# Kernel optimization log

Measured on AMD Instinct MI355X. Metric: run time of the kernel, lower is better.

The kernel has to match this reference:

```python
import math
import jax, jax.numpy as jnp
import numpy as np
from jax import lax

EPS = 1e-6
SAMPLE_RATIO = 0.25
K = 5


def _grid_idx(loc_orig, h, w):
    # loc_orig in [-1,1] -> nearest grid cell flat index (row-major)
    loc = (jnp.clip(loc_orig, -1.0, 1.0) + 1.0) * 0.5
    col = jnp.clip(jnp.round(loc[..., 0] * (w - 1)).astype(jnp.int32), 0, w - 1)
    row = jnp.clip(jnp.round(loc[..., 1] * (h - 1)).astype(jnp.int32), 0, h - 1)
    return row * w + col


def token2map(x, loc_orig, idx_agg, H, W):
    # scatter tokens (via their original points) into an HxW grid, averaging per cell
    B, N, C = x.shape
    N0 = idx_agg.shape[1]
    idx_hw = _grid_idx(loc_orig, H, W)                      # (B, N0)
    tok = jax.vmap(lambda xb, ib: xb[ib])(x, idx_agg)       # (B, N0, C)

    def per_b(ihw, t):
        cnt = jax.ops.segment_sum(jnp.ones((N0,), x.dtype), ihw, num_segments=H * W)
        s = jax.ops.segment_sum(t, ihw, num_segments=H * W)
        return s / (cnt + EPS)[:, None]

    grid = jax.vmap(per_b)(idx_hw, tok)                     # (B, H*W, C)
    return grid.reshape(B, H, W, C).transpose(0, 3, 1, 2)   # (B, C, H, W)


def map2token(x_map, N, loc_orig, idx_agg, agg_weight):
    # gather map values at original points, weighted scatter-reduce back to N tokens
    B, C, h, w = x_map.shape
    idx_hw = _grid_idx(loc_orig, h, w)
    flat = x_map.reshape(B, C, h * w).transpose(0, 2, 1)    # (B, hw, C)
    feat = jax.vmap(lambda fb, ib: fb[ib])(flat, idx_hw)    # (B, N0, C)
    aw = agg_weight[..., 0]                                 # (B, N0)

    def per_b(ia, a, f):
        tot = jax.ops.segment_sum(a, ia, num_segments=N) + EPS
        return jax.ops.segment_sum(f * (a / tot[ia])[:, None], ia, num_segments=N)

    return jax.vmap(per_b)(idx_agg, aw, feat)               # (B, N, C)


def cluster_dpc_knn(x, cluster_num, k):
    # DPC-KNN: density from k-NN distances, parent distance, score = dist*density
    B, N, C = x.shape
    sq = jnp.sum(x * x, -1)
    dist = jnp.sqrt(jnp.maximum(sq[:, :, None] + sq[:, None, :]
                                - 2.0 * jnp.einsum('bnc,bmc->bnm', x, x), 0.0)) / math.sqrt(C)
    neg_near, _ = lax.top_k(-dist, k)                       # k nearest (incl. self, dist 0)
    density = jnp.exp(-jnp.mean(jnp.square(neg_near), -1))  # (B, N)
    mask = density[:, None, :] > density[:, :, None]
    dist_max = jnp.max(dist.reshape(B, -1), -1)[:, None, None]
    d_parent = jnp.min(jnp.where(mask, dist, dist_max), -1)
    score = d_parent * density
    _, index_down = lax.top_k(score, cluster_num)           # (B, M) cluster centers
    dist_down = jax.vmap(lambda db, ib: db[ib])(dist, index_down)  # (B, M, N)
    idx_cluster = jnp.argmin(dist_down, axis=1)             # (B, N)
    b = jnp.arange(B)[:, None]
    idx_cluster = idx_cluster.at[b, index_down].set(jnp.arange(cluster_num)[None, :])
    return idx_cluster


def layer_norm(x, g, b):
    mu = jnp.mean(x, -1, keepdims=True)
    xc = x - mu
    return xc * lax.rsqrt(jnp.mean(xc * xc, -1, keepdims=True) + 1e-5) * g + b


def setup_inputs() -> dict:
    key = jax.random.key(0)
    ks = jax.random.split(key, 8)
    B, N, C, DOUT, H, W = 4, 4096, 128, 256, 64, 64
    return {
        "x": jax.random.normal(ks[0], (B, N, C), jnp.float32),
        "loc_orig": jax.random.uniform(ks[1], (B, N, 2), jnp.float32, minval=-1.0, maxval=1.0),
        "idx_agg": jax.random.randint(ks[2], (B, N), 0, N),
        "agg_weight": jax.random.uniform(ks[3], (B, N, 1), jnp.float32),
        "H": H,
        "W": W,
        "idx_k_loc": jax.random.randint(ks[4], (B, N, K), 0, N),
        "conv_w": jax.random.normal(ks[5], (DOUT, C, 3, 3), jnp.float32) * 0.02,
        "conv_b": jnp.zeros((DOUT,), jnp.float32),
        "skip_w": jax.random.normal(ks[6], (DOUT, C), jnp.float32) * 0.02,
        "ln_g": jnp.ones((DOUT,), jnp.float32),
        "ln_b": jnp.zeros((DOUT,), jnp.float32),
        "conf_w": jax.random.normal(ks[7], (1, DOUT), jnp.float32) * 0.02,
        "conf_b": jnp.zeros((1,), jnp.float32),
    }


def reference(x, loc_orig, idx_agg, agg_weight, H, W, idx_k_loc,
              conv_w, conv_b, skip_w, ln_g, ln_b, conf_w, conf_b):
    B, N, C = x.shape
    x_map = token2map(x, loc_orig, idx_agg, H, W)           # (B, C, H, W)
    x_map = lax.conv_general_dilated(x_map, conv_w, (2, 2), ((1, 1), (1, 1)),
                                     dimension_numbers=('NCHW', 'OIHW', 'NCHW'))
    x_map = x_map + conv_b[None, :, None, None]             # (B, DOUT, H/2, W/2)
    xt = map2token(x_map, N, loc_orig, idx_agg, agg_weight) + x @ skip_w.T
    xt = layer_norm(xt, ln_g, ln_b)
    conf = xt @ conf_w.T + conf_b                           # (B, N, 1)
    weight = jnp.exp(conf)[..., 0]                          # (B, N)
    M = max(int(math.ceil(N * SAMPLE_RATIO)), 1)
    idx_cluster = cluster_dpc_knn(xt, M, K)                 # (B, N)

    def merge_b(ic, wb, xb):
        allw = jax.ops.segment_sum(wb, ic, num_segments=M) + EPS
        nw = wb / allw[ic]
        return jax.ops.segment_sum(xb * nw[:, None], ic, num_segments=M), nw

    x_down, norm_w = jax.vmap(merge_b)(idx_cluster, weight, xt)   # (B, M, DOUT), (B, N)
    idx_agg_down = jax.vmap(lambda ic, ia: ic[ia])(idx_cluster, idx_agg)        # (B, N0)
    weight_t = jax.vmap(lambda nw, ia: nw[ia])(norm_w, idx_agg)[..., None]      # (B, N0, 1)
    agg_weight_down = agg_weight * weight_t
    agg_weight_down = agg_weight_down / jnp.max(agg_weight_down, axis=1, keepdims=True)
    # down_block treated as identity (external module); use_grid=False path -> idx_k_loc_down is None
    return (x_down, idx_agg_down, agg_weight_down)
```

## Files before the change

### kernel.cpp

```cpp
#include <hip/hip_runtime.h>
#include <math.h>

#define NB 4
#define NT 4096
#define CI 128
#define DOUT 256
#define HWI 4096
#define HWO 1024
#define MC 1024
#define EPS_F 1e-6f
#define GSZ 16777216ull
#define GSZB 67108864ull

typedef unsigned short u16;
typedef __attribute__((ext_vector_type(8))) short bf16x8;
typedef __attribute__((ext_vector_type(4))) float f32x4;

static const size_t OFF_XMAP  = 0;
static const size_t OFF_CNT   = OFF_XMAP + 8388608;
static const size_t OFF_TOT   = OFF_CNT  + 65536;
static const size_t OFF_ALLW  = OFF_TOT  + 65536;
static const size_t OFF_VMAX  = OFF_ALLW + 16384;
static const size_t OFF_AWDM  = OFF_VMAX + 256;
static const size_t ZERO_BYTES= OFF_AWDM + 256;
static const size_t OFF_YMAP  = ZERO_BYTES;
static const size_t OFF_XT    = OFF_YMAP + 4194304;
static const size_t OFF_SQ    = OFF_XT + 16777216;
static const size_t OFF_DEN   = OFF_SQ + 65536;
static const size_t OFF_SCORE = OFF_DEN + 65536;
static const size_t OFF_WT    = OFF_SCORE + 65536;
static const size_t OFF_AWD   = OFF_WT + 65536;
static const size_t OFF_IDXD  = OFF_AWD + 65536;
static const size_t OFF_IDXC  = OFF_IDXD + 16384;
static const size_t OFF_INV   = OFF_IDXC + 65536;
static const size_t OFF_WTR   = OFF_INV + 65536;
static const size_t OFF_SWT   = OFF_WTR + 1179648;
static const size_t OFF_P     = OFF_SWT + 131072;
static const size_t OFF_XH    = OFF_P + 18874368;
static const size_t OFF_XM    = OFF_XH + 8388608;
static const size_t OFF_XL    = OFF_XM + 8388608;
static const size_t OFF_G     = OFF_XL + 8388608;
static const size_t DPSTRIDE  = (size_t)NT*32*6;

__device__ __forceinline__ float waveSum(float v){
#pragma unroll
  for (int m = 1; m < 64; m <<= 1) v += __shfl_xor(v, m, 64);
  return v;
}
__device__ __forceinline__ float blockSum256(float v, float* red){
  v = waveSum(v);
  int lane = threadIdx.x & 63, wid = threadIdx.x >> 6;
  __syncthreads();
  if (lane == 0) red[wid] = v;
  __syncthreads();
  return red[0] + red[1] + red[2] + red[3];
}
__device__ __forceinline__ void merge5(float& a0, float& a1, float& a2, float& a3, float& a4,
                                       float b0, float b1, float b2, float b3, float b4){
  float l0=a0,l1=a1,l2=a2,l3=fminf(a3,b4),l4=fminf(a4,b3),l5=b2,l6=b1,l7=b0;
  float t0=fminf(l0,l4), t4=fmaxf(l0,l4);
  float t1=fminf(l1,l5), t5=fmaxf(l1,l5);
  float t2=fminf(l2,l6), t6=fmaxf(l2,l6);
  float t3=fminf(l3,l7), t7=fmaxf(l3,l7);
  float u0=fminf(t0,t2), u2=fmaxf(t0,t2);
  float u1=fminf(t1,t3), u3=fmaxf(t1,t3);
  float u4=fminf(t4,t6);
  float u5=fminf(t5,t7);
  a0=fminf(u0,u1); a1=fmaxf(u0,u1);
  a2=fminf(u2,u3); a3=fmaxf(u2,u3);
  a4=fminf(u4,u5);
}
__device__ __forceinline__ void ins5(float v, float& t0, float& t1, float& t2, float& t3, float& t4){
  t4 = fminf(t4, v);
  float a;
  a = fminf(t3,t4); t4 = fmaxf(t3,t4); t3 = a;
  a = fminf(t2,t3); t3 = fmaxf(t2,t3); t2 = a;
  a = fminf(t1,t2); t2 = fmaxf(t1,t2); t1 = a;
  a = fminf(t0,t1); t1 = fmaxf(t0,t1); t0 = a;
}
__device__ __forceinline__ int grid_cell(float lx, float ly, int dim){
  lx = (fminf(fmaxf(lx, -1.f), 1.f) + 1.f) * 0.5f;
  ly = (fminf(fmaxf(ly, -1.f), 1.f) + 1.f) * 0.5f;
  float s = (float)(dim - 1);
  int col = (int)rintf(lx * s); col = min(max(col, 0), dim - 1);
  int row = (int)rintf(ly * s); row = min(max(row, 0), dim - 1);
  return row * dim + col;
}

__global__ __launch_bounds__(256) void t2m_scatter(const float* __restrict__ x,
                                                   const float* __restrict__ loc,
                                                   const int* __restrict__ idx_agg,
                                                   const float* __restrict__ aggw,
                                                   float* __restrict__ xmap, float* __restrict__ cnt,
                                                   float* __restrict__ tot){
  int lin = blockIdx.x * 256 + threadIdx.x;
  int c  = lin & 127;
  int bn = lin >> 7;
  int b  = bn >> 12;
  float lx = loc[(size_t)bn*2 + 0];
  float ly = loc[(size_t)bn*2 + 1];
  int cell = grid_cell(lx, ly, 64);
  int ia = idx_agg[bn];
  float val = x[((size_t)(b*NT + ia))*CI + c];
  atomicAdd(&xmap[((size_t)(b*HWI + cell))*CI + c], val);
  if (c == 0) atomicAdd(&cnt[b*HWI + cell], 1.0f);
  if (c == 1) atomicAdd(&tot[b*NT + ia], aggw[bn]);
}

__global__ __launch_bounds__(256) void wprep_kernel(const float* __restrict__ cw, const float* __restrict__ sw,
                                                    float* __restrict__ wT, float* __restrict__ swT){
  int lin = blockIdx.x * 256 + threadIdx.x;
  if (lin < 1152*256){
    int k = lin >> 8, d = lin & 255;
    wT[lin] = cw[(size_t)d*1152 + k];
  } else {
    int i = lin - 1152*256;
    int c = i >> 8, d = i & 255;
    swT[i] = sw[d*128 + c];
  }
}

__global__ __launch_bounds__(256) void im2col_kernel(const float* __restrict__ xmap,
                                                     const float* __restrict__ cnt,
                                                     float* __restrict__ P){
  int tid = threadIdx.x;
  int c = tid & 127, n2 = tid >> 7;
  int n = blockIdx.x * 2 + n2;
  int b = n >> 10, rem = n & 1023;
  int oh = rem >> 5, ow = rem & 31;
  const float* xb = xmap + (size_t)b*HWI*CI;
  const float* cb_ = cnt + (size_t)b*HWI;
  float* prow = P + (size_t)n*1152 + c*9;
#pragma unroll
  for (int kh = 0; kh < 3; ++kh){
    int ih = oh*2 - 1 + kh;
#pragma unroll
    for (int kw = 0; kw < 3; ++kw){
      int iw = ow*2 - 1 + kw;
      bool inb = (ih >= 0) && (ih < 64) && (iw >= 0) && (iw < 64);
      float v = 0.f;
      if (inb){
        int cell = ih*64 + iw;
        v = xb[(size_t)cell*CI + c] / (cb_[cell] + EPS_F);
      }
      prow[kh*3 + kw] = v;
    }
  }
}

__global__ __launch_bounds__(256) void conv_gemm(const float* __restrict__ P,
                                                 const float* __restrict__ wT,
                                                 const float* __restrict__ cb,
                                                 float* __restrict__ ymap){
  __shared__ float As[16][64];
  __shared__ float Bs[16][32];
  int n0 = blockIdx.x * 64, d0 = blockIdx.y * 32;
  int tid = threadIdx.x;
  int tx = tid & 15, ty = tid >> 4;
  int ln = tid & 63, kq = tid >> 6;
  int bkr = tid >> 3, bc4 = (tid & 7) * 4;
  float4 pav = *(const float4*)(P + (size_t)(n0+ln)*1152 + kq*4);
  float4 pbv;
  if (tid < 128) pbv = *(const float4*)(wT + (size_t)bkr*256 + d0 + bc4);
  float acc[4][2] = {{0}};
  for (int kt = 0; kt < 72; ++kt){
    __syncthreads();
    As[kq*4+0][ln]=pav.x; As[kq*4+1][ln]=pav.y; As[kq*4+2][ln]=pav.z; As[kq*4+3][ln]=pav.w;
    if (tid < 128) *(float4*)&Bs[bkr][bc4] = pbv;
    __syncthreads();
    if (kt < 71){
      int k2 = (kt + 1) * 16;
      pav = *(const float4*)(P + (size_t)(n0+ln)*1152 + k2 + kq*4);
      if (tid < 128) pbv = *(const float4*)(wT + (size_t)(k2 + bkr)*256 + d0 + bc4);
    }
#pragma unroll
    for (int k = 0; k < 16; ++k){
      float ar[4];
      *(float4*)ar = *(const float4*)&As[k][ty*4];
      float b0 = Bs[k][tx*2], b1 = Bs[k][tx*2+1];
#pragma unroll
      for (int r = 0; r < 4; ++r){ acc[r][0] += ar[r]*b0; acc[r][1] += ar[r]*b1; }
    }
  }
  float c0 = cb[d0 + tx*2], c1 = cb[d0 + tx*2 + 1];
#pragma unroll
  for (int r = 0; r < 4; ++r){
    float2 o; o.x = acc[r][0] + c0; o.y = acc[r][1] + c1;
    *(float2*)(ymap + (size_t)(n0 + ty*4 + r)*DOUT + d0 + tx*2) = o;
  }
}

__global__ __launch_bounds__(256) void skip_kernel(const float* __restrict__ x,
                                                   const float* __restrict__ swT,
                                                   float* __restrict__ xt){
  int rowbase = blockIdx.x * 8;
  int d = threadIdx.x;
  __shared__ float xr[8*128];
  ((float4*)xr)[d] = ((const float4*)(x + (size_t)rowbase*CI))[d];
  __syncthreads();
  float acc[8] = {0,0,0,0,0,0,0,0};
  for (int c = 0; c < 128; ++c){
    float w = swT[c*256 + d];
#pragma unroll
    for (int r = 0; r < 8; ++r) acc[r] += w * xr[r*128 + c];
  }
  for (int r = 0; r < 8; ++r) xt[(size_t)(rowbase + r)*DOUT + d] = acc[r];
}

__global__ __launch_bounds__(256) void m2t_scatter(const float* __restrict__ ymap,
                                                   const float* __restrict__ loc,
                                                   const int* __restrict__ idx_agg,
                                                   const float* __restrict__ aggw,
                                                   const float* __restrict__ tot,
                                                   float* __restrict__ xt){
  int bn = blockIdx.x;
  int d = threadIdx.x;
  int b = bn >> 12;
  float lx = loc[(size_t)bn*2 + 0];
  float ly = loc[(size_t)bn*2 + 1];
  int cell = grid_cell(lx, ly, 32);
  int ia = idx_agg[bn];
  float w = aggw[bn] / (tot[b*NT + ia] + EPS_F);
  float val = ymap[((size_t)(b*HWO + cell))*DOUT + d] * w;
  atomicAdd(&xt[((size_t)(b*NT + ia))*DOUT + d], val);
}

__global__ __launch_bounds__(256) void ln_kernel(float* __restrict__ xt,
                                                 const float* __restrict__ g,
                                                 const float* __restrict__ bta,
                                                 const float* __restrict__ cw,
                                                 const float* __restrict__ cb,
                                                 float* __restrict__ sq, float* __restrict__ wt){
  __shared__ float red[4];
  int row = blockIdx.x;
  int d = threadIdx.x;
  float v = xt[(size_t)row*DOUT + d];
  float mu = blockSum256(v, red) * (1.0f/256.0f);
  float xc = v - mu;
  float var = blockSum256(xc*xc, red) * (1.0f/256.0f);
  float rn = 1.0f / sqrtf(var + 1e-5f);
  float y = xc * rn * g[d] + bta[d];
  xt[(size_t)row*DOUT + d] = y;
  float s2 = blockSum256(y*y, red);
  float cf = blockSum256(y*cw[d], red);
  if (d == 0){ sq[row] = s2; wt[row] = expf(cf + cb[0]); }
}

__global__ __launch_bounds__(256) void xsplit_kernel(const float* __restrict__ xt,
                                                     u16* __restrict__ xh,
                                                     u16* __restrict__ xm,
                                                     u16* __restrict__ xl){
  int idx = blockIdx.x*256 + threadIdx.x;
  float2 v = *(const float2*)(xt + (size_t)idx*2);
  unsigned ph, pm, pl;
  {
    unsigned u = __float_as_uint(v.x);
    unsigned h0 = u >> 16;
    float r1 = v.x - __uint_as_float(u & 0xFFFF0000u);
    unsigned u1 = __float_as_uint(r1);
    unsigned m0 = u1 >> 16;
    float r2 = r1 - __uint_as_float(u1 & 0xFFFF0000u);
    unsigned l0 = __float_as_uint(r2) >> 16;
    unsigned u2 = __float_as_uint(v.y);
    unsigned h1 = u2 >> 16;
    float s1 = v.y - __uint_as_float(u2 & 0xFFFF0000u);
    unsigned u3 = __float_as_uint(s1);
    unsigned m1 = u3 >> 16;
    float s2 = s1 - __uint_as_float(u3 & 0xFFFF0000u);
    unsigned l1 = __float_as_uint(s2) >> 16;
    ph = h0 | (h1 << 16); pm = m0 | (m1 << 16); pl = l0 | (l1 << 16);
  }
  *(unsigned*)(xh + (size_t)idx*2) = ph;
  *(unsigned*)(xm + (size_t)idx*2) = pm;
  *(unsigned*)(xl + (size_t)idx*2) = pl;
}

__global__ __launch_bounds__(256) void gram_mfma(const u16* __restrict__ xh,
                                                 const u16* __restrict__ xm,
                                                 const u16* __restrict__ xl,
                                                 const float* __restrict__ sq,
                                                 float* __restrict__ G,
                                                 float* __restrict__ Dpart,
                                                 int b_base, size_t gstride){
  __shared__ u16 usmem[24576];
  u16* Au = usmem;
  u16* Bu = usmem + 12288;
  int b = b_base + blockIdx.y;
  float* Gb = G + (size_t)blockIdx.y*gstride;
  float* Dp = Dpart + (size_t)blockIdx.y*DPSTRIDE;
  int t = blockIdx.x;
  int ti = 0, accu = 0;
  while (accu + ti + 1 <= t){ accu += ti + 1; ++ti; }
  int tj = t - accu;
  int i0 = ti*128, j0 = tj*128;
  int tid = threadIdx.x;
  int w = tid >> 6, l = tid & 63;
  int lrow = l & 15, lg = l >> 4;
  const size_t base = (size_t)b*NT*256;
  const u16* csrc[3] = {xh, xm, xl};
  const u16* gptr[12];
  u16* lptr[12];
  {
    int ci = 0;
#pragma unroll
    for (int side = 0; side < 2; ++side)
#pragma unroll
      for (int c = 0; c < 3; ++c)
#pragma unroll
        for (int wv = 0; wv < 2; ++wv){
          int win = w + wv*4;
          int s = win*64 + l;
          int r = (s >> 3) * 2;
          int g = s ^ (r & 7);
          if ((g >> 2) != r){ r += 1; g = s ^ (r & 7); }
          int q = g & 3;
          int rowbase = side ? j0 : i0;
          gptr[ci] = csrc[c] + base + (size_t)(rowbase + r)*256 + q*8;
          lptr[ci] = (side ? Bu : Au) + c*4096 + win*512;
          ++ci;
        }
  }
  f32x4 acc[2][8];
  f32x4 z; z[0]=0.f; z[1]=0.f; z[2]=0.f; z[3]=0.f;
#pragma unroll
  for (int mr = 0; mr < 2; ++mr)
#pragma unroll
    for (int n0 = 0; n0 < 8; ++n0) acc[mr][n0] = z;
  for (int kc = 0; kc < 8; ++kc){
    __syncthreads();
#pragma unroll
    for (int ci = 0; ci < 12; ++ci)
      __builtin_amdgcn_global_load_lds((const void*)(gptr[ci] + kc*32),
                                       (void*)lptr[ci], 16, 0, 0);
    __syncthreads();
    bf16x8 af[2][3];
#pragma unroll
    for (int mr = 0; mr < 2; ++mr){
      int row = w*32 + mr*16 + lrow;
      int off = ((row*4 + lg) ^ (row & 7)) * 8;
#pragma unroll
      for (int c = 0; c < 3; ++c)
        af[mr][c] = *(const bf16x8*)(Au + c*4096 + off);
    }
#pragma unroll
    for (int n0 = 0; n0 < 8; ++n0){
      int rowb = n0*16 + lrow;
      int offb = ((rowb*4 + lg) ^ (rowb & 7)) * 8;
      bf16x8 bh = *(const bf16x8*)(Bu + 0*4096 + offb);
      bf16x8 bm = *(const bf16x8*)(Bu + 1*4096 + offb);
      bf16x8 bl = *(const bf16x8*)(Bu + 2*4096 + offb);
#pragma unroll
      for (int mr = 0; mr < 2; ++mr){
        acc[mr][n0] = __builtin_amdgcn_mfma_f32_16x16x32_bf16(af[mr][0], bh, acc[mr][n0], 0, 0, 0);
        acc[mr][n0] = __builtin_amdgcn_mfma_f32_16x16x32_bf16(af[mr][0], bm, acc[mr][n0], 0, 0, 0);
        acc[mr][n0] = __builtin_amdgcn_mfma_f32_16x16x32_bf16(af[mr][1], bh, acc[mr][n0], 0, 0, 0);
        acc[mr][n0] = __builtin_amdgcn_mfma_f32_16x16x32_bf16(af[mr][1], bm, acc[mr][n0], 0, 0, 0);
        acc[mr][n0] = __builtin_amdgcn_mfma_f32_16x16x32_bf16(af[mr][0], bl, acc[mr][n0], 0, 0, 0);
        acc[mr][n0] = __builtin_amdgcn_mfma_f32_16x16x32_bf16(af[mr][2], bh, acc[mr][n0], 0, 0, 0);
      }
    }
  }
  const float* sqb2 = sq + b*NT;
  {
    float sqj_c[8];
#pragma unroll
    for (int n0 = 0; n0 < 8; ++n0) sqj_c[n0] = sqb2[j0 + n0*16 + lrow];
#pragma unroll
    for (int mr = 0; mr < 2; ++mr)
#pragma unroll
      for (int r = 0; r < 4; ++r){
        int row = i0 + w*32 + mr*16 + lg*4 + r;
        float sqi_v = sqb2[row];
        float t0=INFINITY,t1=INFINITY,t2=INFINITY,t3=INFINITY,t4=INFINITY;
        float mx = 0.f;
#pragma unroll
        for (int n0 = 0; n0 < 8; ++n0){
          float v = fmaxf(sqi_v + sqj_c[n0] - 2.0f*acc[mr][n0][r], 0.0f);
          mx = fmaxf(mx, v);
          ins5(v,t0,t1,t2,t3,t4);
        }
#pragma unroll
        for (int m = 1; m < 16; m <<= 1){
          float b0=__shfl_xor(t0,m,64), b1=__shfl_xor(t1,m,64), b2=__shfl_xor(t2,m,64),
                b3=__shfl_xor(t3,m,64), b4=__shfl_xor(t4,m,64);
          merge5(t0,t1,t2,t3,t4,b0,b1,b2,b3,b4);
          mx = fmaxf(mx, __shfl_xor(mx,m,64));
        }
        if (lrow == 0){
          float* dpp = Dp + ((size_t)row*32 + tj)*6;
          dpp[0]=t0; dpp[1]=t1; dpp[2]=t2; dpp[3]=t3; dpp[4]=t4; dpp[5]=mx;
        }
      }
  }
#pragma unroll
  for (int mr = 0; mr < 2; ++mr)
#pragma unroll
    for (int n0 = 0; n0 < 8; ++n0)
#pragma unroll
      for (int r = 0; r < 4; ++r)
        Gb[(size_t)(i0 + w*32 + mr*16 + lg*4 + r)*NT + j0 + n0*16 + lrow] = acc[mr][n0][r];
  if (ti != tj){
    float* T = (float*)usmem;
    int q = tid >> 3, u = tid & 7;
    float sqi_u[16];
#pragma unroll
    for (int e = 0; e < 16; ++e) sqi_u[e] = sqb2[i0 + u*16 + e];
#pragma unroll
    for (int cc = 0; cc < 4; ++cc){
      __syncthreads();
#pragma unroll
      for (int nn = 0; nn < 2; ++nn){
        int n0 = cc*2 + nn;
#pragma unroll
        for (int mr = 0; mr < 2; ++mr)
#pragma unroll
          for (int r = 0; r < 4; ++r)
            T[(nn*16 + lrow)*129 + w*32 + mr*16 + lg*4 + r] = acc[mr][n0][r];
      }
      __syncthreads();
      const float* Trow = &T[q*129 + u*16];
      float* dst = Gb + (size_t)(j0 + cc*32 + q)*NT + i0 + u*16;
      float gv[16];
#pragma unroll
      for (int e = 0; e < 16; ++e) gv[e] = Trow[e];
      float4 o0, o1, o2, o3;
      o0.x=gv[0]; o0.y=gv[1]; o0.z=gv[2]; o0.w=gv[3];
      o1.x=gv[4]; o1.y=gv[5]; o1.z=gv[6]; o1.w=gv[7];
      o2.x=gv[8]; o2.y=gv[9]; o2.z=gv[10]; o2.w=gv[11];
      o3.x=gv[12]; o3.y=gv[13]; o3.z=gv[14]; o3.w=gv[15];
      *(float4*)dst = o0; *(float4*)(dst + 4) = o1;
      *(float4*)(dst + 8) = o2; *(float4*)(dst + 12) = o3;
      {
        int jr = j0 + cc*32 + q;
        float sqj_m = sqb2[jr];
        float t0=INFINITY,t1=INFINITY,t2=INFINITY,t3=INFINITY,t4=INFINITY;
        float mx = 0.f;
#pragma unroll
        for (int e = 0; e < 16; ++e){
          float v = fmaxf(sqj_m + sqi_u[e] - 2.0f*gv[e], 0.0f);
          mx = fmaxf(mx, v);
          ins5(v,t0,t1,t2,t3,t4);
        }
#pragma unroll
        for (int m = 1; m < 8; m <<= 1){
          float b0=__shfl_xor(t0,m,64), b1=__shfl_xor(t1,m,64), b2=__shfl_xor(t2,m,64),
                b3=__shfl_xor(t3,m,64), b4=__shfl_xor(t4,m,64);
          merge5(t0,t1,t2,t3,t4,b0,b1,b2,b3,b4);
          mx = fmaxf(mx, __shfl_xor(mx,m,64));
        }
        if (u == 0){
          float* dpp = Dp + ((size_t)jr*32 + ti)*6;
          dpp[0]=t0; dpp[1]=t1; dpp[2]=t2; dpp[3]=t3; dpp[4]=t4; dpp[5]=mx;
        }
      }
    }
  }
}

__global__ __launch_bounds__(256) void dens_merge(const float* __restrict__ Dpart,
                                                  float* __restrict__ density, int* __restrict__ vmax,
                                                  int b_base){
  int b = b_base + blockIdx.y;
  const float* Dp = Dpart + (size_t)blockIdx.y*DPSTRIDE;
  int row = blockIdx.x*256 + threadIdx.x;
  const float* p = Dp + (size_t)row*32*6;
  float t0=INFINITY,t1=INFINITY,t2=INFINITY,t3=INFINITY,t4=INFINITY;
  float mx = 0.f;
#pragma unroll 4
  for (int tt = 0; tt < 32; ++tt){
    merge5(t0,t1,t2,t3,t4, p[tt*6+0], p[tt*6+1], p[tt*6+2], p[tt*6+3], p[tt*6+4]);
    mx = fmaxf(mx, p[tt*6+5]);
  }
  float d0=sqrtf(t0)*0.0625f, d1=sqrtf(t1)*0.0625f, d2=sqrtf(t2)*0.0625f,
        d3=sqrtf(t3)*0.0625f, d4=sqrtf(t4)*0.0625f;
  float s = d0*d0; s += d1*d1; s += d2*d2; s += d3*d3; s += d4*d4;
  density[b*NT + row] = expf(-(s / 5.0f));
#pragma unroll
  for (int m = 1; m < 64; m <<= 1) mx = fmaxf(mx, __shfl_xor(mx, m, 64));
  if ((threadIdx.x & 63) == 0) atomicMax(vmax + b, __float_as_int(mx));
}

__global__ __launch_bounds__(256) void parent_all(const float* __restrict__ G, size_t gstride,
                                                  const float* __restrict__ sq,
                                                  const float* __restrict__ density, const int* __restrict__ vmax,
                                                  float* __restrict__ score, int b_base){
  int b = b_base + blockIdx.y;
  const float* Gb = G + (size_t)blockIdx.y*gstride;
  int i = blockIdx.x*4 + (threadIdx.x >> 6);
  int lane = threadIdx.x & 63;
  const float* sqb = sq + b*NT;
  const float* den = density + b*NT;
  float sqi = sqb[i];
  float di = den[i];
  const float4* row4 = (const float4*)(Gb + (size_t)i*NT);
  const float4* sq4  = (const float4*)sqb;
  const float4* dn4  = (const float4*)den;
  float4 ga[8], gb2[8];
#pragma unroll
  for (int p = 0; p < 8; ++p) ga[p] = row4[p*64 + lane];
#pragma unroll
  for (int p = 0; p < 8; ++p) gb2[p] = row4[(8+p)*64 + lane];
  float minv = INFINITY;
#pragma unroll
  for (int p = 0; p < 8; ++p){
    float4 g4 = ga[p];
    float4 s4 = sq4[p*64 + lane];
    float4 d4 = dn4[p*64 + lane];
    float v0 = fmaxf(sqi + s4.x - 2.0f*g4.x, 0.0f);
    float v1 = fmaxf(sqi + s4.y - 2.0f*g4.y, 0.0f);
    float v2 = fmaxf(sqi + s4.z - 2.0f*g4.z, 0.0f);
    float v3 = fmaxf(sqi + s4.w - 2.0f*g4.w, 0.0f);
    minv = fminf(minv, (d4.x > di) ? v0 : INFINITY);
    minv = fminf(minv, (d4.y > di) ? v1 : INFINITY);
    minv = fminf(minv, (d4.z > di) ? v2 : INFINITY);
    minv = fminf(minv, (d4.w > di) ? v3 : INFINITY);
  }
#pragma unroll
  for (int p = 0; p < 8; ++p){
    float4 g4 = gb2[p];
    float4 s4 = sq4[(8+p)*64 + lane];
    float4 d4 = dn4[(8+p)*64 + lane];
    float v0 = fmaxf(sqi + s4.x - 2.0f*g4.x, 0.0f);
    float v1 = fmaxf(sqi + s4.y - 2.0f*g4.y, 0.0f);
    float v2 = fmaxf(sqi + s4.z - 2.0f*g4.z, 0.0f);
    float v3 = fmaxf(sqi + s4.w - 2.0f*g4.w, 0.0f);
    minv = fminf(minv, (d4.x > di) ? v0 : INFINITY);
    minv = fminf(minv, (d4.y > di) ? v1 : INFINITY);
    minv = fminf(minv, (d4.z > di) ? v2 : INFINITY);
    minv = fminf(minv, (d4.w > di) ? v3 : INFINITY);
  }
#pragma unroll
  for (int m = 1; m < 64; m <<= 1) minv = fminf(minv, __shfl_xor(minv,m,64));
  if (lane == 0){
    float dmax = sqrtf(__int_as_float(vmax[b])) * 0.0625f;
    float dp = isinf(minv) ? dmax : sqrtf(minv) * 0.0625f;
    score[b*NT + i] = dp * di;
  }
}

__device__ __forceinline__ bool kv_lt(float s1, int a1, float s2, int a2){
  return (s1 > s2) || (s1 == s2 && a1 < a2);
}
#define KV_CMPX(sx,ax,sy,ay,up) do{ bool _l = kv_lt(sx,ax,sy,ay); \
  if (_l != (up)) { float _ts=sx; sx=sy; sy=_ts; int _ta=ax; ax=ay; ay=_ta; } }while(0)
#define KV_TAKE(sx,ax,ps,pa,eqd) do{ bool _keep = kv_lt(sx,ax,ps,pa) == (eqd); \
  if(!_keep){ sx=(ps); ax=(pa); } }while(0)

__global__ __launch_bounds__(1024) void topk_all(const float* __restrict__ score, int* __restrict__ idx_down,
                                                 int* __restrict__ inv, int b_base){
  __shared__ float ss[4096];
  __shared__ int ii[4096];
  int b = b_base + blockIdx.x;
  int t = threadIdx.x;
  float s0,s1,s2,s3; int a0,a1,a2,a3;
  {
    float4 v = *(const float4*)(score + b*NT + 4*t);
    s0=v.x; s1=v.y; s2=v.z; s3=v.w;
    a0=4*t; a1=4*t+1; a2=4*t+2; a3=4*t+3;
    int4 mi; mi.x=-1; mi.y=-1; mi.z=-1; mi.w=-1;
    *(int4*)(inv + b*NT + 4*t) = mi;
  }
  for (int k = 2; k <= 4096; k <<= 1){
    bool upT = ((4*t) & k) == 0;
    for (int j = k >> 1; j >= 256; j >>= 1){
      __syncthreads();
      float4 sv; sv.x=s0; sv.y=s1; sv.z=s2; sv.w=s3;
      int4 av; av.x=a0; av.y=a1; av.z=a2; av.w=a3;
      *(float4*)&ss[4*t] = sv;
      *(int4*)&ii[4*t] = av;
      __syncthreads();
      int pt = t ^ (j >> 2);
      bool eqd = ((t & (j >> 2)) == 0) == upT;
      float4 ps = *(const float4*)&ss[4*pt];
      int4  pa = *(const int4*)&ii[4*pt];
      KV_TAKE(s0,a0,ps.x,pa.x,eqd);
      KV_TAKE(s1,a1,ps.y,pa.y,eqd);
      KV_TAKE(s2,a2,ps.z,pa.z,eqd);
      KV_TAKE(s3,a3,ps.w,pa.w,eqd);
    }
    int jhi = (k >> 1) < 128 ? (k >> 1) : 128;
    for (int j = jhi; j >= 4; j >>= 1){
      int dl = j >> 2;
      bool eqd = ((t & dl) == 0) == upT;
      { float ps=__shfl_xor(s0,dl,64); int pa=__shfl_xor(a0,dl,64); KV_TAKE(s0,a0,ps,pa,eqd); }
      { float ps=__shfl_xor(s1,dl,64); int pa=__shfl_xor(a1,dl,64); KV_TAKE(s1,a1,ps,pa,eqd); }
      { float ps=__shfl_xor(s2,dl,64); int pa=__shfl_xor(a2,dl,64); KV_TAKE(s2,a2,ps,pa,eqd); }
      { float ps=__shfl_xor(s3,dl,64); int pa=__shfl_xor(a3,dl,64); KV_TAKE(s3,a3,ps,pa,eqd); }
    }
    if (k >= 4){
      KV_CMPX(s0,a0,s2,a2,upT);
      KV_CMPX(s1,a1,s3,a3,upT);
      KV_CMPX(s0,a0,s1,a1,upT);
      KV_CMPX(s2,a2,s3,a3,upT);
    } else {
      KV_CMPX(s0,a0,s1,a1,true);
      KV_CMPX(s2,a2,s3,a3,false);
    }
  }
  __syncthreads();
  if (t < 256){
    int tok;
    tok = a0; idx_down[b*MC + 4*t + 0] = tok; inv[b*NT + tok] = 4*t + 0;
    tok = a1; idx_down[b*MC + 4*t + 1] = tok; inv[b*NT + tok] = 4*t + 1;
    tok = a2; idx_down[b*MC + 4*t + 2] = tok; inv[b*NT + tok] = 4*t + 2;
    tok = a3; idx_down[b*MC + 4*t + 3] = tok; inv[b*NT + tok] = 4*t + 3;
  }
}

__global__ __launch_bounds__(256) void assign_all(const float* __restrict__ G, size_t gstride,
                                                  const float* __restrict__ sq,
                                                  const int* __restrict__ idx_down, const int* __restrict__ inv,
                                                  const float* __restrict__ wt,
                                                  int* __restrict__ idx_cluster, float* __restrict__ allw,
                                                  int b_base){
  int b = b_base + blockIdx.y;
  const float* Gb = G + (size_t)blockIdx.y*gstride;
  int jl = threadIdx.x & 15, mq = threadIdx.x >> 4;
  int j = blockIdx.x * 16 + jl;
  const float* sqb = sq + b*NT;
  float sqj = sqb[j];
  const int* idb = idx_down + b*MC;
  float bestd = INFINITY; int bestm = 0x7fffffff;
  for (int m = mq*64; m < mq*64 + 64; ++m){
    int im = idb[m];
    float g = Gb[(size_t)im*NT + j];
    float v = fmaxf(sqb[im] + sqj - 2.0f*g, 0.0f);
    float d = sqrtf(v) * 0.0625f;
    if (d < bestd){ bestd = d; bestm = m; }
  }
  __shared__ float ld[16][17];
  __shared__ int lm[16][17];
  ld[mq][jl] = bestd; lm[mq][jl] = bestm;
  __syncthreads();
  if (mq == 0){
    for (int q = 1; q < 16; ++q){
      float d2 = ld[q][jl]; int m2 = lm[q][jl];
      if (d2 < bestd || (d2 == bestd && m2 < bestm)){ bestd = d2; bestm = m2; }
    }
    int iv = inv[b*NT + j];
    int final_m = (iv >= 0) ? iv : bestm;
    idx_cluster[b*NT + j] = final_m;
    atomicAdd(&allw[b*MC + final_m], wt[b*NT + j]);
  }
}

__global__ __launch_bounds__(256) void xdown_kernel(const int* __restrict__ idx_cluster,
                                                    const float* __restrict__ wt, const float* __restrict__ allw,
                                                    const float* __restrict__ xt, float* __restrict__ out0){
  int bn = blockIdx.x;
  int d = threadIdx.x;
  int b = bn >> 12;
  int ic = idx_cluster[bn];
  float nw = wt[bn] / (allw[b*MC + ic] + EPS_F);
  float v = xt[(size_t)bn*DOUT + d] * nw;
  atomicAdd(&out0[((size_t)(b*MC + ic))*DOUT + d], v);
}
__global__ __launch_bounds__(256) void out12a_kernel(const int* __restrict__ idx_agg, const int* __restrict__ idx_cluster,
                                                     const float* __restrict__ aggw,
                                                     const float* __restrict__ wt, const float* __restrict__ allw,
                                                     float* __restrict__ awd, int* __restrict__ awdmax,
                                                     float* __restrict__ out1){
  __shared__ float red[4];
  int lin = blockIdx.x * 256 + threadIdx.x;
  int b = lin >> 12;
  int ia = idx_agg[lin];
  int ic = idx_cluster[b*NT + ia];
  out1[lin] = (float)ic;
  float nw = wt[b*NT + ia] / (allw[b*MC + ic] + EPS_F);
  float v = aggw[lin] * nw;
  awd[lin] = v;
  float wv = v;
#pragma unroll
  for (int m = 1; m < 64; m <<= 1) wv = fmaxf(wv, __shfl_xor(wv, m, 64));
  int lane = threadIdx.x & 63, wid = threadIdx.x >> 6;
  if (lane == 0) red[wid] = wv;
  __syncthreads();
  if (threadIdx.x == 0){
    float bm = fmaxf(fmaxf(red[0], red[1]), fmaxf(red[2], red[3]));
    atomicMax(&awdmax[b], __float_as_int(bm));
  }
}
__global__ __launch_bounds__(256) void out2_kernel(const float* __restrict__ awd, const int* __restrict__ awdmax,
                                                   float* __restrict__ out2){
  int lin = blockIdx.x * 256 + threadIdx.x;
  int b = lin >> 12;
  out2[lin] = awd[lin] / __int_as_float(awdmax[b]);
}

extern "C" void kernel_launch(void* const* d_in, const int* in_sizes, int n_in,
                              void* d_out, int out_size, void* d_ws, size_t ws_size,
                              hipStream_t stream) {
  const float* x      = (const float*)d_in[0];
  const float* loc    = (const float*)d_in[1];
  const int*   idxagg = (const int*)d_in[2];
  const float* aggw   = (const float*)d_in[3];
  const float* convw  = (const float*)d_in[7];
  const float* convb  = (const float*)d_in[8];
  const float* skipw  = (const float*)d_in[9];
  const float* lng    = (const float*)d_in[10];
  const float* lnb    = (const float*)d_in[11];
  const float* confw  = (const float*)d_in[12];
  const float* confb  = (const float*)d_in[13];

  char* ws = (char*)d_ws;
  float* w_xmap  = (float*)(ws + OFF_XMAP);
  float* w_cnt   = (float*)(ws + OFF_CNT);
  float* w_tot   = (float*)(ws + OFF_TOT);
  float* w_allw  = (float*)(ws + OFF_ALLW);
  int*   w_vmax  = (int*)  (ws + OFF_VMAX);
  int*   w_awdm  = (int*)  (ws + OFF_AWDM);
  float* w_ymap  = (float*)(ws + OFF_YMAP);
  float* w_xt    = (float*)(ws + OFF_XT);
  float* w_sq    = (float*)(ws + OFF_SQ);
  float* w_den   = (float*)(ws + OFF_DEN);
  float* w_score = (float*)(ws + OFF_SCORE);
  float* w_wt    = (float*)(ws + OFF_WT);
  float* w_awd   = (float*)(ws + OFF_AWD);
  int*   w_idxd  = (int*)  (ws + OFF_IDXD);
  int*   w_idxc  = (int*)  (ws + OFF_IDXC);
  int*   w_inv   = (int*)  (ws + OFF_INV);
  float* w_wtr   = (float*)(ws + OFF_WTR);
  float* w_swt   = (float*)(ws + OFF_SWT);
  float* w_p     = (float*)(ws + OFF_P);
  u16*   w_xh    = (u16*)  (ws + OFF_XH);
  u16*   w_xm    = (u16*)  (ws + OFF_XM);
  u16*   w_xl    = (u16*)  (ws + OFF_XL);
  float* w_g     = (float*)(ws + OFF_G);
  float* w_dpart = (float*)(ws + OFF_P);

  int gcount = 1;
  for (int k = 4; k >= 1; --k){
    if (OFF_G + (size_t)k*GSZB <= ws_size){ gcount = k; break; }
  }

  float* out0 = (float*)d_out;
  float* out1 = out0 + NB*MC*DOUT;
  float* out2 = out1 + NB*NT;

  hipMemsetAsync(ws, 0, ZERO_BYTES, stream);
  hipMemsetAsync(out0, 0, (size_t)NB*MC*DOUT*sizeof(float), stream);

  t2m_scatter<<<NB*NT*CI/256, 256, 0, stream>>>(x, loc, idxagg, aggw, w_xmap, w_cnt, w_tot);
  wprep_kernel<<<1280, 256, 0, stream>>>(convw, skipw, w_wtr, w_swt);
  im2col_kernel<<<2048, 256, 0, stream>>>(w_xmap, w_cnt, w_p);
  conv_gemm<<<dim3(64, 8), 256, 0, stream>>>(w_p, w_wtr, convb, w_ymap);
  skip_kernel<<<NB*NT/8, 256, 0, stream>>>(x, w_swt, w_xt);
  m2t_scatter<<<NB*NT, 256, 0, stream>>>(w_ymap, loc, idxagg, aggw, w_tot, w_xt);
  ln_kernel<<<NB*NT, 256, 0, stream>>>(w_xt, lng, lnb, confw, confb, w_sq, w_wt);
  xsplit_kernel<<<NB*NT*DOUT/512, 256, 0, stream>>>(w_xt, w_xh, w_xm, w_xl);

  for (int g0 = 0; g0 < NB; g0 += gcount){
    int gy = (NB - g0 < gcount) ? (NB - g0) : gcount;
    gram_mfma  <<<dim3(528, gy), 256, 0, stream>>>(w_xh, w_xm, w_xl, w_sq, w_g, w_dpart, g0, GSZ);
    dens_merge <<<dim3(16, gy), 256, 0, stream>>>(w_dpart, w_den, w_vmax, g0);
    parent_all <<<dim3(1024, gy), 256, 0, stream>>>(w_g, GSZ, w_sq, w_den, w_vmax, w_score, g0);
    topk_all   <<<gy, 1024, 0, stream>>>(w_score, w_idxd, w_inv, g0);
    assign_all <<<dim3(256, gy), 256, 0, stream>>>(w_g, GSZ, w_sq, w_idxd, w_inv, w_wt, w_idxc, w_allw, g0);
  }

  xdown_kernel<<<NB*NT, 256, 0, stream>>>(w_idxc, w_wt, w_allw, w_xt, out0);
  out12a_kernel<<<NB*NT/256, 256, 0, stream>>>(idxagg, w_idxc, aggw, w_wt, w_allw, w_awd, w_awdm, out1);
  out2_kernel<<<NB*NT/256, 256, 0, stream>>>(w_awd, w_awdm, out2);

  (void)in_sizes; (void)n_in; (void)out_size;
}
```

Before: 612.4 us.

## Exploit Gram symmetry in parent-distance search with triangular tiles

Replaces the row-wise parent-distance kernel with a tiled kernel that visits only lower-triangular 128x128 tiles of the Gram matrix. Each tile computes both row and column masked minima, and a small merge kernel reduces the 32 partial minima per row. This roughly halves global reads of the large Gram matrix. In exchange it adds an extra launch, a partial buffer and a shared-memory column reduction.

```diff
diff --git a/kernel.cpp b/kernel.cpp
--- a/kernel.cpp
+++ b/kernel.cpp
@@ -41,6 +41,8 @@
 static const size_t OFF_XL    = OFF_XM + 8388608;
 static const size_t OFF_G     = OFF_XL + 8388608;
 static const size_t DPSTRIDE  = (size_t)NT*32*6;
+static const size_t OFF_PP    = OFF_P + 4*DPSTRIDE*4;
+static const size_t PPSTRIDE  = (size_t)NT*32;
 
 __device__ __forceinline__ float waveSum(float v){
 #pragma unroll
@@ -480,62 +482,88 @@
   if ((threadIdx.x & 63) == 0) atomicMax(vmax + b, __float_as_int(mx));
 }
 
-__global__ __launch_bounds__(256) void parent_all(const float* __restrict__ G, size_t gstride,
-                                                  const float* __restrict__ sq,
-                                                  const float* __restrict__ density, const int* __restrict__ vmax,
-                                                  float* __restrict__ score, int b_base){
+__global__ __launch_bounds__(256) void parent_tile(const float* __restrict__ G, size_t gstride,
+                                                   const float* __restrict__ sq,
+                                                   const float* __restrict__ density,
+                                                   float* __restrict__ Ppart, int b_base){
+  __shared__ float cs[16][128];
   int b = b_base + blockIdx.y;
   const float* Gb = G + (size_t)blockIdx.y*gstride;
-  int i = blockIdx.x*4 + (threadIdx.x >> 6);
-  int lane = threadIdx.x & 63;
+  float* Pp = Ppart + (size_t)blockIdx.y*PPSTRIDE;
+  int t = blockIdx.x;
+  int ti = 0, accu = 0;
+  while (accu + ti + 1 <= t){ accu += ti + 1; ++ti; }
+  int tj = t - accu;
+  int i0 = ti*128, j0 = tj*128;
+  int tid = threadIdx.x;
+  int tx = tid & 15, ty = tid >> 4;
   const float* sqb = sq + b*NT;
   const float* den = density + b*NT;
-  float sqi = sqb[i];
-  float di = den[i];
-  const float4* row4 = (const float4*)(Gb + (size_t)i*NT);
-  const float4* sq4  = (const float4*)sqb;
-  const float4* dn4  = (const float4*)den;
-  float4 ga[8], gb2[8];
-#pragma unroll
-  for (int p = 0; p < 8; ++p) ga[p] = row4[p*64 + lane];
-#pragma unroll
-  for (int p = 0; p < 8; ++p) gb2[p] = row4[(8+p)*64 + lane];
-  float minv = INFINITY;
-#pragma unroll
-  for (int p = 0; p < 8; ++p){
-    float4 g4 = ga[p];
-    float4 s4 = sq4[p*64 + lane];
-    float4 d4 = dn4[p*64 + lane];
-    float v0 = fmaxf(sqi + s4.x - 2.0f*g4.x, 0.0f);
-    float v1 = fmaxf(sqi + s4.y - 2.0f*g4.y, 0.0f);
-    float v2 = fmaxf(sqi + s4.z - 2.0f*g4.z, 0.0f);
-    float v3 = fmaxf(sqi + s4.w - 2.0f*g4.w, 0.0f);
-    minv = fminf(minv, (d4.x > di) ? v0 : INFINITY);
-    minv = fminf(minv, (d4.y > di) ? v1 : INFINITY);
-    minv = fminf(minv, (d4.z > di) ? v2 : INFINITY);
-    minv = fminf(minv, (d4.w > di) ? v3 : INFINITY);
-  }
-#pragma unroll
-  for (int p = 0; p < 8; ++p){
-    float4 g4 = gb2[p];
-    float4 s4 = sq4[(8+p)*64 + lane];
-    float4 d4 = dn4[(8+p)*64 + lane];
-    float v0 = fmaxf(sqi + s4.x - 2.0f*g4.x, 0.0f);
-    float v1 = fmaxf(sqi + s4.y - 2.0f*g4.y, 0.0f);
-    float v2 = fmaxf(sqi + s4.z - 2.0f*g4.z, 0.0f);
-    float v3 = fmaxf(sqi + s4.w - 2.0f*g4.w, 0.0f);
-    minv = fminf(minv, (d4.x > di) ? v0 : INFINITY);
-    minv = fminf(minv, (d4.y > di) ? v1 : INFINITY);
-    minv = fminf(minv, (d4.z > di) ? v2 : INFINITY);
-    minv = fminf(minv, (d4.w > di) ? v3 : INFINITY);
-  }
-#pragma unroll
-  for (int m = 1; m < 64; m <<= 1) minv = fminf(minv, __shfl_xor(minv,m,64));
-  if (lane == 0){
-    float dmax = sqrtf(__int_as_float(vmax[b])) * 0.0625f;
-    float dp = isinf(minv) ? dmax : sqrtf(minv) * 0.0625f;
-    score[b*NT + i] = dp * di;
-  }
+  float sqi[8], di[8], sqj[8], dj[8];
+#pragma unroll
+  for (int rr = 0; rr < 8; ++rr){
+    int r = i0 + ty*8 + rr;
+    sqi[rr] = sqb[r]; di[rr] = den[r];
+  }
+#pragma unroll
+  for (int cc = 0; cc < 8; ++cc){
+    int c = j0 + tx*8 + cc;
+    sqj[cc] = sqb[c]; dj[cc] = den[c];
+  }
+  float rmin[8], cmin[8];
+#pragma unroll
+  for (int k = 0; k < 8; ++k){ rmin[k] = INFINITY; cmin[k] = INFINITY; }
+#pragma unroll
+  for (int rr = 0; rr < 8; ++rr){
+    int row = i0 + ty*8 + rr;
+    const float4* gp = (const float4*)(Gb + (size_t)row*NT + j0 + tx*8);
+    float4 g0 = gp[0], g1 = gp[1];
+    float gv[8];
+    gv[0]=g0.x; gv[1]=g0.y; gv[2]=g0.z; gv[3]=g0.w;
+    gv[4]=g1.x; gv[5]=g1.y; gv[6]=g1.z; gv[7]=g1.w;
+#pragma unroll
+    for (int cc = 0; cc < 8; ++cc){
+      float v = fmaxf(sqi[rr] + sqj[cc] - 2.0f*gv[cc], 0.0f);
+      rmin[rr] = fminf(rmin[rr], (dj[cc] > di[rr]) ? v : INFINITY);
+      cmin[cc] = fminf(cmin[cc], (di[rr] > dj[cc]) ? v : INFINITY);
+    }
+  }
+#pragma unroll
+  for (int m = 1; m < 16; m <<= 1)
+#pragma unroll
+    for (int rr = 0; rr < 8; ++rr)
+      rmin[rr] = fminf(rmin[rr], __shfl_xor(rmin[rr], m, 64));
+  if (tx == 0){
+#pragma unroll
+    for (int rr = 0; rr < 8; ++rr)
+      Pp[(size_t)(i0 + ty*8 + rr)*32 + tj] = rmin[rr];
+  }
+  if (ti != tj){
+#pragma unroll
+    for (int cc = 0; cc < 8; ++cc) cs[ty][tx*8 + cc] = cmin[cc];
+    __syncthreads();
+    if (tid < 128){
+      float mn = INFINITY;
+#pragma unroll
+      for (int y = 0; y < 16; ++y) mn = fminf(mn, cs[y][tid]);
+      Pp[(size_t)(j0 + tid)*32 + ti] = mn;
+    }
+  }
+}
+
+__global__ __launch_bounds__(256) void parent_merge(const float* __restrict__ Ppart,
+                                                    const float* __restrict__ density,
+                                                    const int* __restrict__ vmax,
+                                                    float* __restrict__ score, int b_base){
+  int b = b_base + blockIdx.y;
+  int row = blockIdx.x*256 + threadIdx.x;
+  const float* p = Ppart + (size_t)blockIdx.y*PPSTRIDE + (size_t)row*32;
+  float mn = INFINITY;
+#pragma unroll 4
+  for (int tt = 0; tt < 32; ++tt) mn = fminf(mn, p[tt]);
+  float dmax = sqrtf(__int_as_float(vmax[b])) * 0.0625f;
+  float dp = isinf(mn) ? dmax : sqrtf(mn) * 0.0625f;
+  score[b*NT + row] = dp * density[b*NT + row];
 }
 
 __device__ __forceinline__ bool kv_lt(float s1, int a1, float s2, int a2){
@@ -727,6 +755,7 @@
   u16*   w_xl    = (u16*)  (ws + OFF_XL);
   float* w_g     = (float*)(ws + OFF_G);
   float* w_dpart = (float*)(ws + OFF_P);
+  float* w_ppart = (float*)(ws + OFF_PP);
 
   int gcount = 1;
   for (int k = 4; k >= 1; --k){
@@ -751,11 +780,12 @@
 
   for (int g0 = 0; g0 < NB; g0 += gcount){
     int gy = (NB - g0 < gcount) ? (NB - g0) : gcount;
-    gram_mfma  <<<dim3(528, gy), 256, 0, stream>>>(w_xh, w_xm, w_xl, w_sq, w_g, w_dpart, g0, GSZ);
-    dens_merge <<<dim3(16, gy), 256, 0, stream>>>(w_dpart, w_den, w_vmax, g0);
-    parent_all <<<dim3(1024, gy), 256, 0, stream>>>(w_g, GSZ, w_sq, w_den, w_vmax, w_score, g0);
-    topk_all   <<<gy, 1024, 0, stream>>>(w_score, w_idxd, w_inv, g0);
-    assign_all <<<dim3(256, gy), 256, 0, stream>>>(w_g, GSZ, w_sq, w_idxd, w_inv, w_wt, w_idxc, w_allw, g0);
+    gram_mfma   <<<dim3(528, gy), 256, 0, stream>>>(w_xh, w_xm, w_xl, w_sq, w_g, w_dpart, g0, GSZ);
+    dens_merge  <<<dim3(16, gy), 256, 0, stream>>>(w_dpart, w_den, w_vmax, g0);
+    parent_tile <<<dim3(528, gy), 256, 0, stream>>>(w_g, GSZ, w_sq, w_den, w_ppart, g0);
+    parent_merge<<<dim3(16, gy), 256, 0, stream>>>(w_ppart, w_den, w_vmax, w_score, g0);
+    topk_all    <<<gy, 1024, 0, stream>>>(w_score, w_idxd, w_inv, g0);
+    assign_all  <<<dim3(256, gy), 256, 0, stream>>>(w_g, GSZ, w_sq, w_idxd, w_inv, w_wt, w_idxc, w_allw, g0);
   }
 
   xdown_kernel<<<NB*NT, 256, 0, stream>>>(w_idxc, w_wt, w_allw, w_xt, out0);
```

Result: no change. 622.9 us (+1.7%).
